# Kernel tuning notes

Measured on AMD Instinct MI355X. Metric: run time of the kernel, lower is better.

## Reference

```python
import jax, jax.numpy as jnp
import numpy as np

B, T, C, N = 64, 1024, 2, 128


def setup_inputs() -> dict:
    key = jax.random.key(0)
    k1, k2, k3, k4, k5 = jax.random.split(key, 5)
    return {
        "emissions": jax.random.normal(k1, (B, T, C, N), dtype=jnp.float32),
        "lengths": jax.random.randint(k2, (B,), T // 2, T + 1),
        "transitions": jax.random.normal(k3, (1, C, N, N), dtype=jnp.float32) * 0.01,
        "start_transitions": jax.random.normal(k4, (1, C, N), dtype=jnp.float32) * 0.01,
        "end_transitions": jax.random.normal(k5, (1, C, N), dtype=jnp.float32) * 0.01,
    }


def reference(emissions, lengths, transitions, start_transitions, end_transitions):
    """CRF log-partition over ragged batch (equivalent to torchlatent's
    log-semiring tree-reduce over PackedSequence, expressed as a masked scan).
    emissions: [B,T,C,N], lengths: [B], transitions: [1,C,N,N],
    start/end_transitions: [1,C,N]. Returns log Z: [B,C].
    """
    trans = transitions[0]              # [C,N,N], shared across time
    alpha0 = start_transitions[0][None] + emissions[:, 0]  # [B,C,N]

    def step(alpha, inp):
        emit, t = inp                   # emit: [B,C,N]
        # log-semiring bmm: logsumexp over previous tag axis
        scores = alpha[:, :, :, None] + trans[None] + emit[:, :, None, :]  # [B,C,N,N]
        new = jax.nn.logsumexp(scores, axis=2)                             # [B,C,N]
        alpha = jnp.where((t < lengths)[:, None, None], new, alpha)
        return alpha, None

    emits = jnp.moveaxis(emissions[:, 1:], 1, 0)  # [T-1,B,C,N]
    alpha, _ = jax.lax.scan(step, alpha0, (emits, jnp.arange(1, T)))
    return jax.nn.logsumexp(alpha + end_transitions[0][None], axis=-1)  # [B,C]
```

## Files before the change

kernel.cpp:

```cpp
#include <hip/hip_runtime.h>

#define BB 64
#define TT 1024
#define CC 2
#define NN 128

#define REP16(M) M(0)M(1)M(2)M(3)M(4)M(5)M(6)M(7)M(8)M(9)M(10)M(11)M(12)M(13)M(14)M(15)

static __device__ __forceinline__ unsigned f2bf(float x) {
    const unsigned u = __float_as_uint(x);
    return (u + 0x7FFFu + ((u >> 16) & 1u)) >> 16;
}
static __device__ __forceinline__ unsigned pk2(float lo, float hi) {
    return f2bf(lo) | (f2bf(hi) << 16);
}

#define DOT(acc, pp, ee) \
    asm("v_dot2_f32_bf16 %0, %1, %2, %0" : "+v"(acc) : "v"(pp), "v"(ee));

#define E_INIT(c) \
    unsigned ue##c##_0 = pk2(__expf(tr[(8*(c)+0)*NN + j]), __expf(tr[(8*(c)+1)*NN + j])); \
    unsigned ue##c##_1 = pk2(__expf(tr[(8*(c)+2)*NN + j]), __expf(tr[(8*(c)+3)*NN + j])); \
    unsigned ue##c##_2 = pk2(__expf(tr[(8*(c)+4)*NN + j]), __expf(tr[(8*(c)+5)*NN + j])); \
    unsigned ue##c##_3 = pk2(__expf(tr[(8*(c)+6)*NN + j]), __expf(tr[(8*(c)+7)*NN + j]));

#define E_PIN(c) \
    asm volatile("" : "+v"(ue##c##_0), "+v"(ue##c##_1), "+v"(ue##c##_2), "+v"(ue##c##_3));

#define MV(c) { const uint4 q = pb[c]; \
    DOT(a0, q.x, ue##c##_0) DOT(a1, q.y, ue##c##_1) \
    DOT(a2, q.z, ue##c##_2) DOT(a3, q.w, ue##c##_3) }

__global__ __launch_bounds__(128, 1) __attribute__((amdgpu_waves_per_eu(1, 1)))
void crf_logz_kernel(const float* __restrict__ emissions,
                     const int* __restrict__ lengths,
                     const float* __restrict__ transitions,
                     const float* __restrict__ start_trans,
                     const float* __restrict__ end_trans,
                     float* __restrict__ out)
{
    const int bc = blockIdx.x;
    const int b  = bc >> 1;
    const int c  = bc & 1;
    const int j  = threadIdx.x;

    __shared__ __align__(16) unsigned short pbufs[2][NN];
    __shared__ float shbuf[2];
    __shared__ float red[NN];

    const float* tr = transitions + c * NN * NN;
    REP16(E_INIT)
    REP16(E_PIN)

    const int len  = lengths[b];
    const int tmax = len - 1;

    const float* emisb = emissions + ((size_t)b * TT * CC + c) * NN;

    float alpha = start_trans[c * NN + j] + emisb[j];
    float shift = 0.f;

    const int t1 = (1 < tmax) ? 1 : tmax, t2 = (2 < tmax) ? 2 : tmax;
    float ecur = emisb[(size_t)t1 * (CC * NN) + j];
    float enx  = emisb[(size_t)t2 * (CC * NN) + j];

    for (int t = 1; t < len; ++t) {
        const int tp = (t + 2 <= tmax) ? (t + 2) : tmax;
        const float el = emisb[(size_t)tp * (CC * NN) + j];

        const float p = __expf(alpha - shift);
        pbufs[t & 1][j] = (unsigned short)f2bf(p);
        if (j == 0) shbuf[t & 1] = alpha;
        __syncthreads();
        const float nshift = shbuf[t & 1];

        const uint4* __restrict__ pb = (const uint4*)pbufs[t & 1];
        float a0 = 0.f, a1 = 0.f, a2 = 0.f, a3 = 0.f;
        REP16(MV)

        alpha = shift + __logf((a0 + a1) + (a2 + a3)) + ecur;
        shift = nshift;
        ecur  = enx; enx = el;
    }

    red[j] = alpha + end_trans[c * NN + j];
    __syncthreads();
    if (j < 64) {
        const float x = red[j], y = red[j + 64];
        float m = fmaxf(x, y);
        #pragma unroll
        for (int off = 32; off > 0; off >>= 1)
            m = fmaxf(m, __shfl_xor(m, off));
        float s = __expf(x - m) + __expf(y - m);
        #pragma unroll
        for (int off = 32; off > 0; off >>= 1)
            s += __shfl_xor(s, off);
        if (j == 0) out[b * CC + c] = m + __logf(s);
    }
}

extern "C" void kernel_launch(void* const* d_in, const int* in_sizes, int n_in,
                              void* d_out, int out_size, void* d_ws, size_t ws_size,
                              hipStream_t stream) {
    const float* emissions   = (const float*)d_in[0];
    const int*   lengths     = (const int*)d_in[1];
    const float* transitions = (const float*)d_in[2];
    const float* start_t     = (const float*)d_in[3];
    const float* end_t       = (const float*)d_in[4];
    float* out = (float*)d_out;

    crf_logz_kernel<<<BB * CC, NN, 0, stream>>>(
        emissions, lengths, transitions, start_t, end_t, out);
}
```

Measured before the change: 542.4 us.

## Shorten per-step critical path by carrying scaled probabilities instead of log alpha

```diff
diff --git a/kernel.cpp b/kernel.cpp
--- a/kernel.cpp
+++ b/kernel.cpp
@@ -31,6 +31,12 @@
     DOT(a0, q.x, ue##c##_0) DOT(a1, q.y, ue##c##_1) \
     DOT(a2, q.z, ue##c##_2) DOT(a3, q.w, ue##c##_3) }
 
+static __device__ __forceinline__ void wg_barrier() {
+    asm volatile("s_waitcnt lgkmcnt(0)" ::: "memory");
+    __builtin_amdgcn_s_barrier();
+    asm volatile("" ::: "memory");
+}
+
 __global__ __launch_bounds__(128, 1) __attribute__((amdgpu_waves_per_eu(1, 1)))
 void crf_logz_kernel(const float* __restrict__ emissions,
                      const int* __restrict__ lengths,
@@ -57,31 +63,42 @@
 
     const float* emisb = emissions + ((size_t)b * TT * CC + c) * NN;
 
-    float alpha = start_trans[c * NN + j] + emisb[j];
-    float shift = 0.f;
+    const float alpha0 = start_trans[c * NN + j] + emisb[j];
+    if (j == 0) shbuf[0] = alpha0;
+
+    unsigned pbits = f2bf(__expf(alpha0));
+    float Scur = 0.f;
 
     const int t1 = (1 < tmax) ? 1 : tmax, t2 = (2 < tmax) ? 2 : tmax;
     float ecur = emisb[(size_t)t1 * (CC * NN) + j];
     float enx  = emisb[(size_t)t2 * (CC * NN) + j];
 
+    float s = 0.f, Sfin = 0.f, efin = ecur;
+
     for (int t = 1; t < len; ++t) {
+        pbufs[t & 1][j] = (unsigned short)pbits;
+        wg_barrier();
+
         const int tp = (t + 2 <= tmax) ? (t + 2) : tmax;
         const float el = emisb[(size_t)tp * (CC * NN) + j];
 
-        const float p = __expf(alpha - shift);
-        pbufs[t & 1][j] = (unsigned short)f2bf(p);
-        if (j == 0) shbuf[t & 1] = alpha;
-        __syncthreads();
-        const float nshift = shbuf[t & 1];
+        const float Snxt = shbuf[(t - 1) & 1];
+        const float f = __expf(Scur + ecur - Snxt);
 
         const uint4* __restrict__ pb = (const uint4*)pbufs[t & 1];
         float a0 = 0.f, a1 = 0.f, a2 = 0.f, a3 = 0.f;
         REP16(MV)
+        s = (a0 + a1) + (a2 + a3);
 
-        alpha = shift + __logf((a0 + a1) + (a2 + a3)) + ecur;
-        shift = nshift;
-        ecur  = enx; enx = el;
+        if (j == 0) shbuf[t & 1] = Scur + __logf(s) + ecur;
+
+        pbits = f2bf(s * f);
+
+        Sfin = Scur; efin = ecur;
+        Scur = Snxt; ecur = enx; enx = el;
     }
+
+    const float alpha = (tmax == 0) ? alpha0 : (Sfin + __logf(s) + efin);
 
     red[j] = alpha + end_trans[c * NN + j];
     __syncthreads();
@@ -91,11 +108,11 @@
         #pragma unroll
         for (int off = 32; off > 0; off >>= 1)
             m = fmaxf(m, __shfl_xor(m, off));
-        float s = __expf(x - m) + __expf(y - m);
+        float ssum = __expf(x - m) + __expf(y - m);
         #pragma unroll
         for (int off = 32; off > 0; off >>= 1)
-            s += __shfl_xor(s, off);
-        if (j == 0) out[b * CC + c] = m + __logf(s);
+            ssum += __shfl_xor(ssum, off);
+        if (j == 0) out[b * CC + c] = m + __logf(ssum);
     }
 }
 
```

Measured after the change: 557.7 us. 1.03x slower.
